# Kernel tuning notes

Measured on AMD Instinct MI355X. Metric: run time of the kernel, lower is better.

## Reference

```python
import jax, jax.numpy as jnp
import numpy as np

NUM_CAPSULES = 16
IN_DIM = 512
OUT_DIM = 32
ROUTING_ITERS = 3
EPS = 1e-08


def setup_inputs() -> dict:
    key = jax.random.key(0)
    kx, kw = jax.random.split(key)
    x = jax.random.normal(kx, (32768, IN_DIM), dtype=jnp.float32)
    W = jax.random.normal(kw, (IN_DIM, NUM_CAPSULES * OUT_DIM), dtype=jnp.float32)
    return {"x": x, "W": W}


def squash(s):
    # s: [batch, out_dim]
    norm = jnp.sum(s * s, axis=-1, keepdims=True)
    scale = norm / (1.0 + norm)
    return scale * s / (jnp.sqrt(norm) + EPS)


def reference(x, W):
    batch = x.shape[0]
    # u: [batch, num_capsules, out_dim]
    u = jnp.matmul(x, W).reshape(batch, NUM_CAPSULES, OUT_DIM)
    b = jnp.zeros((batch, NUM_CAPSULES), dtype=x.dtype)
    v = None
    for _ in range(ROUTING_ITERS):
        c = jax.nn.softmax(b, axis=1)[..., None]       # [batch, caps, 1]
        s = jnp.sum(c * u, axis=1)                      # [batch, out_dim]
        v = squash(s)                                   # [batch, out_dim]
        b = b + jnp.sum(u * v[:, None, :], axis=-1)     # [batch, caps]
    return v
```

## Files before the change

### kernel.cpp

```cpp
#include <hip/hip_runtime.h>
#include <math.h>


#define BATCH   32768
#define KDIM    512
#define NDIM    512
#define OUT_DIM 32
#define EPS_F   1e-8f
#define NKT     32

typedef _Float16 half8  __attribute__((ext_vector_type(8)));
typedef float   floatx4 __attribute__((ext_vector_type(4)));
typedef float  floatx16 __attribute__((ext_vector_type(16)));

template <int CTRL>
__device__ __forceinline__ float dpp_mov(float x) {
    return __int_as_float(__builtin_amdgcn_mov_dpp(__float_as_int(x), CTRL, 0xF, 0xF, true));
}
template <int XMASK>
__device__ __forceinline__ float swz_xor(float x) {
    return __int_as_float(__builtin_amdgcn_ds_swizzle(__float_as_int(x), (XMASK << 10) | 31));
}
#define ROR4  0x124
#define ROR8  0x128
#define QXOR1 0xB1
#define QXOR2 0x4E

__device__ __forceinline__ float cap_sum(float x) {
    x += dpp_mov<ROR4>(x);
    x += dpp_mov<ROR8>(x);
    x += swz_xor<16>(x);
    x += __shfl_xor(x, 32);
    return x;
}
__device__ __forceinline__ float cap_max(float x) {
    x = fmaxf(x, dpp_mov<ROR4>(x));
    x = fmaxf(x, dpp_mov<ROR8>(x));
    x = fmaxf(x, swz_xor<16>(x));
    x = fmaxf(x, __shfl_xor(x, 32));
    return x;
}
__device__ __forceinline__ float dg_sum(float x) {
    x += dpp_mov<QXOR1>(x);
    x += dpp_mov<QXOR2>(x);
    return x;
}

__global__ void prep_w(const float* __restrict__ W, _Float16* __restrict__ Wh,
                       _Float16* __restrict__ Wl) {
    __shared__ float tile[32][33];
    const int tx = threadIdx.x, ty = threadIdx.y;
    const int n0 = blockIdx.x * 32, k0 = blockIdx.y * 32;
#pragma unroll
    for (int i = 0; i < 4; ++i)
        tile[ty + 8 * i][tx] = W[(size_t)(k0 + ty + 8 * i) * NDIM + n0 + tx];
    __syncthreads();
#pragma unroll
    for (int i = 0; i < 4; ++i) {
        const int k = k0 + tx, n = n0 + ty + 8 * i;
        const float v = tile[tx][ty + 8 * i];
        const _Float16 h = (_Float16)v;
        const _Float16 l = (_Float16)(v - (float)h);
        const size_t off = (size_t)(k >> 4) * (NDIM * 16) + (size_t)n * 16 + (k & 15);
        Wh[off] = h;
        Wl[off] = l;
    }
}

__device__ __forceinline__ void ld_g2l_16(void* lds_base_uniform, const void* g) {
    __builtin_amdgcn_global_load_lds(
        (const __attribute__((address_space(1))) void*)g,
        (__attribute__((address_space(3))) void*)lds_base_uniform, 16, 0, 0);
}

__global__ __launch_bounds__(512, 2)
void capsule_mfma(const float* __restrict__ x, const _Float16* __restrict__ Wh,
                  const _Float16* __restrict__ Wl, float* __restrict__ out) {
    __shared__ __align__(16) char smem[66560];
    _Float16 (*Bs)[2][NDIM][16] = (_Float16 (*)[2][NDIM][16])smem;
    float (*u_lds)[520] = (float (*)[520])smem;

    const int tid  = threadIdx.x;
    const int w    = tid >> 6;
    const int lane = tid & 63;
    const int r = w >> 2, c = w & 3;
    const int ln = lane & 31, q = lane >> 5;
    const int rowBlk = blockIdx.x * 128;
    const int R0 = rowBlk + r * 64;
    const int C0 = c * 128;

    floatx16 acc[2][4];
#pragma unroll
    for (int mf = 0; mf < 2; ++mf)
#pragma unroll
        for (int nt = 0; nt < 4; ++nt)
#pragma unroll
            for (int i = 0; i < 16; ++i) acc[mf][nt][i] = 0.f;

    const float* aptr0 = x + (size_t)(R0 + ln) * KDIM + q * 8;
    const float* aptr1 = aptr0 + (size_t)32 * KDIM;

    const int nseg = w * 64;

    ld_g2l_16(&Bs[0][0][nseg][0],      Wh + (size_t)nseg * 16 + lane * 8);
    ld_g2l_16(&Bs[0][0][nseg + 32][0], Wh + (size_t)(nseg + 32) * 16 + lane * 8);
    ld_g2l_16(&Bs[0][1][nseg][0],      Wl + (size_t)nseg * 16 + lane * 8);
    ld_g2l_16(&Bs[0][1][nseg + 32][0], Wl + (size_t)(nseg + 32) * 16 + lane * 8);
    floatx4 a[2][2];
    a[0][0] = *(const floatx4*)(aptr0);
    a[0][1] = *(const floatx4*)(aptr0 + 4);
    a[1][0] = *(const floatx4*)(aptr1);
    a[1][1] = *(const floatx4*)(aptr1 + 4);

#pragma unroll 2
    for (int kt = 0; kt < NKT; ++kt) {
        __syncthreads();
        const int buf = kt & 1;
        if (kt + 1 < NKT) {
            const size_t g = (size_t)(kt + 1) * (NDIM * 16);
            ld_g2l_16(&Bs[buf ^ 1][0][nseg][0],      Wh + g + (size_t)nseg * 16 + lane * 8);
            ld_g2l_16(&Bs[buf ^ 1][0][nseg + 32][0], Wh + g + (size_t)(nseg + 32) * 16 + lane * 8);
            ld_g2l_16(&Bs[buf ^ 1][1][nseg][0],      Wl + g + (size_t)nseg * 16 + lane * 8);
            ld_g2l_16(&Bs[buf ^ 1][1][nseg + 32][0], Wl + g + (size_t)(nseg + 32) * 16 + lane * 8);
        }
        floatx4 pr[2][2];
        if (kt + 1 < NKT) {
            pr[0][0] = *(const floatx4*)(aptr0 + (kt + 1) * 16);
            pr[0][1] = *(const floatx4*)(aptr0 + (kt + 1) * 16 + 4);
            pr[1][0] = *(const floatx4*)(aptr1 + (kt + 1) * 16);
            pr[1][1] = *(const floatx4*)(aptr1 + (kt + 1) * 16 + 4);
        }
        half8 ah[2], al[2];
#pragma unroll
        for (int mf = 0; mf < 2; ++mf) {
            const float av[8] = {a[mf][0][0], a[mf][0][1], a[mf][0][2], a[mf][0][3],
                                 a[mf][1][0], a[mf][1][1], a[mf][1][2], a[mf][1][3]};
#pragma unroll
            for (int j = 0; j < 8; ++j) {
                const _Float16 h = (_Float16)av[j];
                ah[mf][j] = h;
                al[mf][j] = (_Float16)(av[j] - (float)h);
            }
        }
#pragma unroll
        for (int nt = 0; nt < 4; ++nt) {
            const half8 bh = *(const half8*)&Bs[buf][0][C0 + nt * 32 + ln][q * 8];
            const half8 bl = *(const half8*)&Bs[buf][1][C0 + nt * 32 + ln][q * 8];
#pragma unroll
            for (int mf = 0; mf < 2; ++mf) {
                acc[mf][nt] = __builtin_amdgcn_mfma_f32_32x32x16_f16(ah[mf], bh, acc[mf][nt], 0, 0, 0);
                acc[mf][nt] = __builtin_amdgcn_mfma_f32_32x32x16_f16(al[mf], bh, acc[mf][nt], 0, 0, 0);
                acc[mf][nt] = __builtin_amdgcn_mfma_f32_32x32x16_f16(ah[mf], bl, acc[mf][nt], 0, 0, 0);
            }
        }
        if (kt + 1 < NKT) {
#pragma unroll
            for (int mf = 0; mf < 2; ++mf) { a[mf][0] = pr[mf][0]; a[mf][1] = pr[mf][1]; }
        }
    }

    const int dgrp = lane & 3;
#pragma unroll
    for (int p = 0; p < 4; ++p) {
        __syncthreads();
        if (r == (p >> 1)) {
            const int mf = p & 1;
#pragma unroll
            for (int nt = 0; nt < 4; ++nt)
#pragma unroll
                for (int reg = 0; reg < 16; ++reg)
                    u_lds[(reg & 3) + 8 * (reg >> 2) + 4 * q][C0 + nt * 32 + ln] = acc[mf][nt][reg];
        }
        __syncthreads();
#pragma unroll 1
        for (int ri = 0; ri < 4; ++ri) {
            const int rl = w * 4 + ri;
            const floatx4 ua = *(const floatx4*)&u_lds[rl][lane * 8];
            const floatx4 ub = *(const floatx4*)&u_lds[rl][lane * 8 + 4];
            const float u8[8] = {ua[0], ua[1], ua[2], ua[3],
                                 ub[0], ub[1], ub[2], ub[3]};
            float b_own = 0.f;
            float v[8];
#pragma unroll
            for (int it = 0; it < 3; ++it) {
                float c_own;
                if (it == 0) {
                    c_own = 1.0f / 16.0f;
                } else {
                    const float m = cap_max(b_own);
                    const float e = __expf(b_own - m);
                    const float ssum = cap_sum(e);
                    c_own = e / ssum;
                }
                float s[8];
#pragma unroll
                for (int j = 0; j < 8; ++j) s[j] = c_own * u8[j];
#pragma unroll
                for (int j = 0; j < 8; ++j) s[j] += dpp_mov<ROR4>(s[j]);
#pragma unroll
                for (int j = 0; j < 8; ++j) s[j] += dpp_mov<ROR8>(s[j]);
#pragma unroll
                for (int j = 0; j < 8; ++j) s[j] += swz_xor<16>(s[j]);
#pragma unroll
                for (int j = 0; j < 8; ++j) s[j] += __shfl_xor(s[j], 32);
                float nrm = 0.f;
#pragma unroll
                for (int j = 0; j < 8; ++j) nrm = fmaf(s[j], s[j], nrm);
                nrm = dg_sum(nrm);
                const float scale = nrm / ((1.f + nrm) * (sqrtf(nrm) + EPS_F));
#pragma unroll
                for (int j = 0; j < 8; ++j) v[j] = scale * s[j];
                if (it < 2) {
                    float dot = 0.f;
#pragma unroll
                    for (int j = 0; j < 8; ++j) dot = fmaf(u8[j], v[j], dot);
                    dot = dg_sum(dot);
                    b_own += dot;
                }
            }
            if (lane < 4) {
                float4* o = (float4*)(out + (size_t)(rowBlk + p * 32 + rl) * OUT_DIM
                                      + dgrp * 8);
                o[0] = make_float4(v[0], v[1], v[2], v[3]);
                o[1] = make_float4(v[4], v[5], v[6], v[7]);
            }
        }
    }
}

extern "C" void kernel_launch(void* const* d_in, const int* in_sizes, int n_in,
                              void* d_out, int out_size, void* d_ws, size_t ws_size,
                              hipStream_t stream) {
    const float* x = (const float*)d_in[0];
    const float* W = (const float*)d_in[1];
    float* out = (float*)d_out;
    _Float16* Wh = (_Float16*)d_ws;
    _Float16* Wl = Wh + (size_t)NDIM * KDIM;

    prep_w<<<dim3(16, 16), dim3(32, 8), 0, stream>>>(W, Wh, Wl);
    capsule_mfma<<<dim3(BATCH / 128), dim3(512), 0, stream>>>(x, Wh, Wl, out);
}
```

Measured before the change: 167.6 us.

## Stage split-fp16 A tile through double-buffered swizzled LDS shared by column warps

Each block now loads its 128-row slice of x into LDS once per k-step. Every thread loads and converts one float4 into fp16 hi/lo pairs, writing them into a double-buffered, XOR-swizzled A tile. Before, each of the four column warps loaded the same rows from global memory and redid the hi/lo split. Sharing the tile is meant to cut that redundant global traffic and conversion work by four, at the cost of extra LDS reads and writes, and LDS per block grows to 80 KB, which could limit occupancy.

```diff
diff --git a/kernel.cpp b/kernel.cpp
--- a/kernel.cpp
+++ b/kernel.cpp
@@ -10,6 +10,7 @@
 #define NKT     32
 
 typedef _Float16 half8  __attribute__((ext_vector_type(8)));
+typedef _Float16 half4t __attribute__((ext_vector_type(4)));
 typedef float   floatx4 __attribute__((ext_vector_type(4)));
 typedef float  floatx16 __attribute__((ext_vector_type(16)));
 
@@ -73,10 +74,12 @@
         (__attribute__((address_space(3))) void*)lds_base_uniform, 16, 0, 0);
 }
 
+#define AS_OFF 65536
+
 __global__ __launch_bounds__(512, 2)
 void capsule_mfma(const float* __restrict__ x, const _Float16* __restrict__ Wh,
                   const _Float16* __restrict__ Wl, float* __restrict__ out) {
-    __shared__ __align__(16) char smem[66560];
+    __shared__ __align__(16) char smem[81920];
     _Float16 (*Bs)[2][NDIM][16] = (_Float16 (*)[2][NDIM][16])smem;
     float (*u_lds)[520] = (float (*)[520])smem;
 
@@ -86,7 +89,6 @@
     const int r = w >> 2, c = w & 3;
     const int ln = lane & 31, q = lane >> 5;
     const int rowBlk = blockIdx.x * 128;
-    const int R0 = rowBlk + r * 64;
     const int C0 = c * 128;
 
     floatx16 acc[2][4];
@@ -97,50 +99,59 @@
 #pragma unroll
             for (int i = 0; i < 16; ++i) acc[mf][nt][i] = 0.f;
 
-    const float* aptr0 = x + (size_t)(R0 + ln) * KDIM + q * 8;
-    const float* aptr1 = aptr0 + (size_t)32 * KDIM;
+    const int srow = tid >> 2;
+    const int skq  = tid & 3;
+    const float* sga = x + (size_t)(rowBlk + srow) * KDIM + skq * 4;
+    const int ssw = (srow >> 1) & 3;
+    const int swoff_h = srow * 64 + (((skq >> 1) ^ ssw) * 16) + (skq & 1) * 8;
+    const int swoff_l = srow * 64 + ((((skq >> 1) ^ 2) ^ ssw) * 16) + (skq & 1) * 8;
+
+    int afr_h[2], afr_l[2];
+#pragma unroll
+    for (int mf = 0; mf < 2; ++mf) {
+        const int ar = r * 64 + mf * 32 + ln;
+        const int asw = (ar >> 1) & 3;
+        afr_h[mf] = ar * 64 + ((q ^ asw) * 16);
+        afr_l[mf] = ar * 64 + (((q ^ 2) ^ asw) * 16);
+    }
 
     const int nseg = w * 64;
 
+    {
+        const floatx4 v0 = *(const floatx4*)sga;
+        half4t h4, l4;
+#pragma unroll
+        for (int j = 0; j < 4; ++j) {
+            h4[j] = (_Float16)v0[j];
+            l4[j] = (_Float16)(v0[j] - (float)h4[j]);
+        }
+        *(half4t*)(smem + AS_OFF + swoff_h) = h4;
+        *(half4t*)(smem + AS_OFF + swoff_l) = l4;
+    }
     ld_g2l_16(&Bs[0][0][nseg][0],      Wh + (size_t)nseg * 16 + lane * 8);
     ld_g2l_16(&Bs[0][0][nseg + 32][0], Wh + (size_t)(nseg + 32) * 16 + lane * 8);
     ld_g2l_16(&Bs[0][1][nseg][0],      Wl + (size_t)nseg * 16 + lane * 8);
     ld_g2l_16(&Bs[0][1][nseg + 32][0], Wl + (size_t)(nseg + 32) * 16 + lane * 8);
-    floatx4 a[2][2];
-    a[0][0] = *(const floatx4*)(aptr0);
-    a[0][1] = *(const floatx4*)(aptr0 + 4);
-    a[1][0] = *(const floatx4*)(aptr1);
-    a[1][1] = *(const floatx4*)(aptr1 + 4);
 
 #pragma unroll 2
     for (int kt = 0; kt < NKT; ++kt) {
         __syncthreads();
         const int buf = kt & 1;
+        floatx4 sv;
         if (kt + 1 < NKT) {
             const size_t g = (size_t)(kt + 1) * (NDIM * 16);
             ld_g2l_16(&Bs[buf ^ 1][0][nseg][0],      Wh + g + (size_t)nseg * 16 + lane * 8);
             ld_g2l_16(&Bs[buf ^ 1][0][nseg + 32][0], Wh + g + (size_t)(nseg + 32) * 16 + lane * 8);
             ld_g2l_16(&Bs[buf ^ 1][1][nseg][0],      Wl + g + (size_t)nseg * 16 + lane * 8);
             ld_g2l_16(&Bs[buf ^ 1][1][nseg + 32][0], Wl + g + (size_t)(nseg + 32) * 16 + lane * 8);
-        }
-        floatx4 pr[2][2];
-        if (kt + 1 < NKT) {
-            pr[0][0] = *(const floatx4*)(aptr0 + (kt + 1) * 16);
-            pr[0][1] = *(const floatx4*)(aptr0 + (kt + 1) * 16 + 4);
-            pr[1][0] = *(const floatx4*)(aptr1 + (kt + 1) * 16);
-            pr[1][1] = *(const floatx4*)(aptr1 + (kt + 1) * 16 + 4);
-        }
+            sv = *(const floatx4*)(sga + (kt + 1) * 16);
+        }
+        const int abase = AS_OFF + buf * 8192;
         half8 ah[2], al[2];
 #pragma unroll
         for (int mf = 0; mf < 2; ++mf) {
-            const float av[8] = {a[mf][0][0], a[mf][0][1], a[mf][0][2], a[mf][0][3],
-                                 a[mf][1][0], a[mf][1][1], a[mf][1][2], a[mf][1][3]};
-#pragma unroll
-            for (int j = 0; j < 8; ++j) {
-                const _Float16 h = (_Float16)av[j];
-                ah[mf][j] = h;
-                al[mf][j] = (_Float16)(av[j] - (float)h);
-            }
+            ah[mf] = *(const half8*)(smem + abase + afr_h[mf]);
+            al[mf] = *(const half8*)(smem + abase + afr_l[mf]);
         }
 #pragma unroll
         for (int nt = 0; nt < 4; ++nt) {
@@ -154,8 +165,15 @@
             }
         }
         if (kt + 1 < NKT) {
-#pragma unroll
-            for (int mf = 0; mf < 2; ++mf) { a[mf][0] = pr[mf][0]; a[mf][1] = pr[mf][1]; }
+            half4t h4, l4;
+#pragma unroll
+            for (int j = 0; j < 4; ++j) {
+                h4[j] = (_Float16)sv[j];
+                l4[j] = (_Float16)(sv[j] - (float)h4[j]);
+            }
+            const int nbase = AS_OFF + (buf ^ 1) * 8192;
+            *(half4t*)(smem + nbase + swoff_h) = h4;
+            *(half4t*)(smem + nbase + swoff_l) = l4;
         }
     }
 
```

New measurement: 157.0 us. 6.3% less time.
